# Kernel optimization log

Measured on AMD Instinct MI355X. Metric: run time of the kernel, lower is better.

Reference implementation:

```python
import jax, jax.numpy as jnp
import numpy as np

NUM_USER = 1_000_000
NUM_ITEM = 100_000
LATENT_DIM = 64
NUM_PARTITIONS = 4
NUM_CENTROIDS = 256
CLUSTER_DIM = LATENT_DIM // NUM_PARTITIONS  # 16
BATCH = 4096
N_NEG = 200


def setup_inputs() -> dict:
    key = jax.random.key(0)
    ks = jax.random.split(key, 7)
    user_id = jax.random.randint(ks[0], (BATCH,), 0, NUM_USER)
    pos_id = jax.random.randint(ks[1], (BATCH, 1), 0, NUM_ITEM)
    neg_ids = jax.random.randint(ks[2], (BATCH, N_NEG), 0, NUM_ITEM)
    # learned parameters
    user_table = jax.random.normal(ks[3], (NUM_USER, LATENT_DIM), jnp.float32) * 0.1
    centroids = jax.random.normal(ks[4], (NUM_PARTITIONS, NUM_CENTROIDS, CLUSTER_DIM), jnp.float32) * 0.1
    item_table = jax.random.normal(ks[5], (NUM_ITEM, LATENT_DIM), jnp.float32) * 0.1
    # pre-sampled uniform noise for the gumbel-softmax (one per partition/user/centroid)
    eps = 1e-10
    gumbel_u = jnp.clip(jax.random.uniform(ks[6], (NUM_PARTITIONS, BATCH, NUM_CENTROIDS), jnp.float32), eps, 1.0 - eps)
    return {
        "user_id": user_id,
        "pos_id": pos_id,
        "neg_ids": neg_ids,
        "user_table": user_table,
        "centroids": centroids,
        "item_table": item_table,
        "gumbel_u": gumbel_u,
    }


def _encode_user(user_emb, centroids, gumbel_u):
    # user_emb: [B, D]; centroids: [P, K, C]; gumbel_u: [P, B, K]
    B = user_emb.shape[0]
    P, K, C = centroids.shape
    ue = user_emb.reshape(B, P, C)  # split latent dim into P partitions
    # squared euclidean distance per partition: [B, P, K]
    dist = ((ue ** 2).sum(-1)[..., None]
            + (centroids ** 2).sum(-1)[None, :, :]
            - 2.0 * jnp.einsum('bpc,pkc->bpk', ue, centroids))
    neg_dist = -dist  # logits fed to softmax / gumbel-softmax
    logits = jax.nn.softmax(neg_dist, axis=-1)  # [B, P, K] (self.logits, transposed)
    # gumbel-softmax, tau=1, hard=True (straight-through)
    gumbels = -jnp.log(-jnp.log(gumbel_u))  # [P, B, K]
    y_soft = jax.nn.softmax(neg_dist + jnp.transpose(gumbels, (1, 0, 2)), axis=-1)
    y_hard = jax.nn.one_hot(jnp.argmax(y_soft, axis=-1), K, dtype=y_soft.dtype)
    idx_center = y_hard + y_soft - jax.lax.stop_gradient(y_soft)  # [B, P, K]
    encode = jnp.einsum('bpk,pkc->bpc', idx_center, centroids).reshape(B, P * C)  # [B, D]
    return encode, logits


def reference(user_id, pos_id, neg_ids, user_table, centroids, item_table, gumbel_u):
    user_emb = user_table[user_id]                       # [B, D] gather
    user_vec, _logits = _encode_user(user_emb, centroids, gumbel_u)
    user_vecs = user_vec[:, None, :]                     # [B, 1, D]
    pos_items = item_table[pos_id]                       # [B, 1, D]
    neg_items = item_table[neg_ids]                      # [B, N, D]
    pos_scores = (user_vecs * pos_items).sum(-1)         # [B, 1]
    neg_scores = (user_vecs * neg_items).sum(-1)         # [B, N]
    return (pos_scores, neg_scores)
```

## Files before the change

kernel.cpp:

```cpp
#include <hip/hip_runtime.h>

#define BATCH 4096
#define NNEG  200
#define NITEM 201
#define DIM   64
#define NPART 4
#define NCENT 256
#define CDIM  16
#define CPAD  17

__global__ __launch_bounds__(256) void qvae_encode_kernel(
    const int*   __restrict__ user_id,
    const float* __restrict__ user_table,
    const float* __restrict__ centroids,
    const float* __restrict__ gumbel_u,
    float*       __restrict__ user_vec)
{
    __shared__ float cent[NCENT * CPAD];

    const int p    = blockIdx.y;
    const int tid  = threadIdx.x;
    const int w    = tid >> 6;
    const int lane = tid & 63;
    const int b    = blockIdx.x * 4 + w;

    const float* cp = centroids + (size_t)p * NCENT * CDIM;
    for (int idx = tid; idx < NCENT * CDIM; idx += 256) {
        int row = idx >> 4, col = idx & 15;
        cent[row * CPAD + col] = cp[idx];
    }
    __syncthreads();
    {
        float s = 0.f;
        #pragma unroll
        for (int c = 0; c < CDIM; ++c) { float v = cent[tid * CPAD + c]; s += v * v; }
        cent[tid * CPAD + CDIM] = s;
    }
    __syncthreads();

    const int uid = user_id[b];
    const float* up = user_table + (size_t)uid * DIM + p * CDIM;
    float ue[CDIM];
    #pragma unroll
    for (int i = 0; i < 4; ++i) {
        float4 v = ((const float4*)up)[i];
        ue[4*i+0] = v.x; ue[4*i+1] = v.y; ue[4*i+2] = v.z; ue[4*i+3] = v.w;
    }
    float ue2 = 0.f;
    #pragma unroll
    for (int c = 0; c < CDIM; ++c) ue2 += ue[c] * ue[c];

    const float* gp = gumbel_u + ((size_t)p * BATCH + b) * NCENT;
    float best_s = -INFINITY;
    int   best_k = 0;
    #pragma unroll
    for (int j = 0; j < 4; ++j) {
        const int k = j * 64 + lane;
        float u = gp[k];
        float g = -logf(-logf(u));
        float dot = 0.f, c2 = cent[k * CPAD + CDIM];
        #pragma unroll
        for (int c = 0; c < CDIM; ++c) dot += ue[c] * cent[k * CPAD + c];
        float dist = (ue2 + c2) - 2.0f * dot;
        float s = -dist + g;
        if (s > best_s) { best_s = s; best_k = k; }
    }

    #pragma unroll
    for (int m = 1; m < 64; m <<= 1) {
        float so = __shfl_xor(best_s, m, 64);
        int   ko = __shfl_xor(best_k, m, 64);
        if (so > best_s || (so == best_s && ko < best_k)) { best_s = so; best_k = ko; }
    }

    if (lane < CDIM) {
        user_vec[(size_t)b * DIM + p * CDIM + lane] = cent[best_k * CPAD + lane];
    }
}

__global__ __launch_bounds__(256) void qvae_score_kernel(
    const int*   __restrict__ pos_id,
    const int*   __restrict__ neg_ids,
    const float* __restrict__ item_table,
    const float* __restrict__ user_vec,
    float*       __restrict__ out)
{
    __shared__ float4 uv4[DIM / 4];
    __shared__ int    ids[NITEM];
    __shared__ float  res[NITEM];

    const int b   = blockIdx.x;
    const int tid = threadIdx.x;

    if (tid < DIM / 4) uv4[tid] = ((const float4*)(user_vec + (size_t)b * DIM))[tid];
    if (tid == 0)           ids[0]   = pos_id[b];
    else if (tid <= NNEG)   ids[tid] = neg_ids[(size_t)b * NNEG + tid - 1];
    __syncthreads();

    const int grp = tid >> 4;
    const int l16 = tid & 15;
    const float4 u = uv4[l16];

    for (int item = grp; item < NITEM; item += 16) {
        const float4 v = ((const float4*)(item_table + (size_t)ids[item] * DIM))[l16];
        float s = v.x * u.x + v.y * u.y + v.z * u.z + v.w * u.w;
        s += __shfl_xor(s, 1, 64);
        s += __shfl_xor(s, 2, 64);
        s += __shfl_xor(s, 4, 64);
        s += __shfl_xor(s, 8, 64);
        if (l16 == 0) res[item] = s;
    }
    __syncthreads();

    if (tid == 0)   out[b] = res[0];
    if (tid < NNEG) out[BATCH + (size_t)b * NNEG + tid] = res[tid + 1];
}

extern "C" void kernel_launch(void* const* d_in, const int* in_sizes, int n_in,
                              void* d_out, int out_size, void* d_ws, size_t ws_size,
                              hipStream_t stream) {
    const int*   user_id    = (const int*)  d_in[0];
    const int*   pos_id     = (const int*)  d_in[1];
    const int*   neg_ids    = (const int*)  d_in[2];
    const float* user_table = (const float*)d_in[3];
    const float* centroids  = (const float*)d_in[4];
    const float* item_table = (const float*)d_in[5];
    const float* gumbel_u   = (const float*)d_in[6];
    float* out = (float*)d_out;
    float* uv  = (float*)d_ws;

    qvae_encode_kernel<<<dim3(BATCH / 4, NPART), 256, 0, stream>>>(
        user_id, user_table, centroids, gumbel_u, uv);
    qvae_score_kernel<<<BATCH, 256, 0, stream>>>(
        pos_id, neg_ids, item_table, uv, out);
}
```

Baseline: 357.0 us.

## Fuse user encoding and item scoring into a single per-user kernel

Merges the encode and score kernels into one launch, with one block per user and each wavefront handling one partition. The quantized user vector now stays in shared memory instead of going through a global workspace. Centroids are read directly from global memory (L2/L1-cached), with norms recomputed per use, rather than staged in LDS. This removes a launch and a global round trip, at the cost of redundant centroid loads and norm computation in every block.

```diff
diff --git a/kernel.cpp b/kernel.cpp
--- a/kernel.cpp
+++ b/kernel.cpp
@@ -7,62 +7,59 @@
 #define NPART 4
 #define NCENT 256
 #define CDIM  16
-#define CPAD  17
 
-__global__ __launch_bounds__(256) void qvae_encode_kernel(
+__global__ __launch_bounds__(256) void qvae_fused_kernel(
     const int*   __restrict__ user_id,
+    const int*   __restrict__ pos_id,
+    const int*   __restrict__ neg_ids,
     const float* __restrict__ user_table,
     const float* __restrict__ centroids,
+    const float* __restrict__ item_table,
     const float* __restrict__ gumbel_u,
-    float*       __restrict__ user_vec)
+    float*       __restrict__ out)
 {
-    __shared__ float cent[NCENT * CPAD];
+    __shared__ float uvs[DIM];
+    __shared__ int   ids[NITEM];
+    __shared__ float res[NITEM];
 
-    const int p    = blockIdx.y;
+    const int b    = blockIdx.x;
     const int tid  = threadIdx.x;
     const int w    = tid >> 6;
     const int lane = tid & 63;
-    const int b    = blockIdx.x * 4 + w;
-
-    const float* cp = centroids + (size_t)p * NCENT * CDIM;
-    for (int idx = tid; idx < NCENT * CDIM; idx += 256) {
-        int row = idx >> 4, col = idx & 15;
-        cent[row * CPAD + col] = cp[idx];
-    }
-    __syncthreads();
-    {
-        float s = 0.f;
-        #pragma unroll
-        for (int c = 0; c < CDIM; ++c) { float v = cent[tid * CPAD + c]; s += v * v; }
-        cent[tid * CPAD + CDIM] = s;
-    }
-    __syncthreads();
 
     const int uid = user_id[b];
-    const float* up = user_table + (size_t)uid * DIM + p * CDIM;
+
+    const float4* up4 = (const float4*)(user_table + (size_t)uid * DIM + w * CDIM);
     float ue[CDIM];
     #pragma unroll
     for (int i = 0; i < 4; ++i) {
-        float4 v = ((const float4*)up)[i];
+        float4 v = up4[i];
         ue[4*i+0] = v.x; ue[4*i+1] = v.y; ue[4*i+2] = v.z; ue[4*i+3] = v.w;
     }
     float ue2 = 0.f;
     #pragma unroll
     for (int c = 0; c < CDIM; ++c) ue2 += ue[c] * ue[c];
 
-    const float* gp = gumbel_u + ((size_t)p * BATCH + b) * NCENT;
+    const float*  gp  = gumbel_u + ((size_t)w * BATCH + b) * NCENT;
+    const float4* cb4 = (const float4*)(centroids + (size_t)w * NCENT * CDIM);
+
     float best_s = -INFINITY;
     int   best_k = 0;
     #pragma unroll
     for (int j = 0; j < 4; ++j) {
         const int k = j * 64 + lane;
-        float u = gp[k];
-        float g = -logf(-logf(u));
-        float dot = 0.f, c2 = cent[k * CPAD + CDIM];
+        float cr[CDIM];
         #pragma unroll
-        for (int c = 0; c < CDIM; ++c) dot += ue[c] * cent[k * CPAD + c];
-        float dist = (ue2 + c2) - 2.0f * dot;
-        float s = -dist + g;
+        for (int i = 0; i < 4; ++i) {
+            float4 v = cb4[k * 4 + i];
+            cr[4*i+0] = v.x; cr[4*i+1] = v.y; cr[4*i+2] = v.z; cr[4*i+3] = v.w;
+        }
+        float c2 = 0.f, dot = 0.f;
+        #pragma unroll
+        for (int c = 0; c < CDIM; ++c) { c2 += cr[c] * cr[c]; dot += ue[c] * cr[c]; }
+        const float u = gp[k];
+        const float g = -logf(-logf(u));
+        const float s = -((ue2 + c2) - 2.0f * dot) + g;
         if (s > best_s) { best_s = s; best_k = k; }
     }
 
@@ -74,36 +71,20 @@
     }
 
     if (lane < CDIM) {
-        user_vec[(size_t)b * DIM + p * CDIM + lane] = cent[best_k * CPAD + lane];
+        uvs[w * CDIM + lane] = centroids[((size_t)w * NCENT + best_k) * CDIM + lane];
     }
-}
 
-__global__ __launch_bounds__(256) void qvae_score_kernel(
-    const int*   __restrict__ pos_id,
-    const int*   __restrict__ neg_ids,
-    const float* __restrict__ item_table,
-    const float* __restrict__ user_vec,
-    float*       __restrict__ out)
-{
-    __shared__ float4 uv4[DIM / 4];
-    __shared__ int    ids[NITEM];
-    __shared__ float  res[NITEM];
-
-    const int b   = blockIdx.x;
-    const int tid = threadIdx.x;
-
-    if (tid < DIM / 4) uv4[tid] = ((const float4*)(user_vec + (size_t)b * DIM))[tid];
-    if (tid == 0)           ids[0]   = pos_id[b];
-    else if (tid <= NNEG)   ids[tid] = neg_ids[(size_t)b * NNEG + tid - 1];
+    if (tid == 0)         ids[0]   = pos_id[b];
+    else if (tid <= NNEG) ids[tid] = neg_ids[(size_t)b * NNEG + tid - 1];
     __syncthreads();
 
     const int grp = tid >> 4;
     const int l16 = tid & 15;
-    const float4 u = uv4[l16];
+    const float4 u4 = ((const float4*)uvs)[l16];
 
     for (int item = grp; item < NITEM; item += 16) {
         const float4 v = ((const float4*)(item_table + (size_t)ids[item] * DIM))[l16];
-        float s = v.x * u.x + v.y * u.y + v.z * u.z + v.w * u.w;
+        float s = v.x * u4.x + v.y * u4.y + v.z * u4.z + v.w * u4.w;
         s += __shfl_xor(s, 1, 64);
         s += __shfl_xor(s, 2, 64);
         s += __shfl_xor(s, 4, 64);
@@ -127,10 +108,7 @@
     const float* item_table = (const float*)d_in[5];
     const float* gumbel_u   = (const float*)d_in[6];
     float* out = (float*)d_out;
-    float* uv  = (float*)d_ws;
 
-    qvae_encode_kernel<<<dim3(BATCH / 4, NPART), 256, 0, stream>>>(
-        user_id, user_table, centroids, gumbel_u, uv);
-    qvae_score_kernel<<<BATCH, 256, 0, stream>>>(
-        pos_id, neg_ids, item_table, uv, out);
+    qvae_fused_kernel<<<BATCH, 256, 0, stream>>>(
+        user_id, pos_id, neg_ids, user_table, centroids, item_table, gumbel_u, out);
 }
```

New measurement: 395.9 us. 10.9% more time.
